# Kernel optimization log

Hardware: AMD Instinct MI355X
Metric: run time of the kernel (lower is better)

The kernel has to match this reference:

```python
import jax, jax.numpy as jnp
import numpy as np

# FIR kernel from resample_kernel=(1,3,3,1): outer product, normalized (gain=1)
_FIR_1D = np.array([1.0, 3.0, 3.0, 1.0], dtype=np.float32)
_FIR = np.outer(_FIR_1D, _FIR_1D)
_FIR = _FIR / _FIR.sum()  # 4x4


def setup_inputs() -> dict:
    key = jax.random.key(0)
    k1, k2, k3 = jax.random.split(key, 3)
    x = jax.random.normal(k1, (16, 256, 64, 64), dtype=jnp.float32)
    # fan_avg uniform init (default_init): variance = 1/fan_avg, fan_in=fan_out=256*9
    scale = float(np.sqrt(3.0 / (256 * 9)))
    w = jax.random.uniform(k2, (256, 256, 3, 3), dtype=jnp.float32, minval=-scale, maxval=scale)
    b = jax.random.normal(k3, (256,), dtype=jnp.float32) * 0.01
    return {"x": x, "w": w, "b": b}


def reference(x, w, b):
    # conv_downsample_2d: upfirdn2d(x, k, pad=(2,2)) then conv2d stride 2, then + bias
    B, C, H, W = x.shape
    # upfirdn2d with up=1, down=1 == zero-padded true convolution with k.
    # k is symmetric so flip is a no-op, but keep it for faithfulness.
    fir = jnp.asarray(_FIR[::-1, ::-1])                       # [4,4]
    fir_k = jnp.tile(fir[None, None, :, :], (C, 1, 1, 1))     # [C,1,4,4] depthwise
    x = jax.lax.conv_general_dilated(
        x, fir_k,
        window_strides=(1, 1),
        padding=((2, 2), (2, 2)),                             # (p+1)//2, p//2 with p=4
        feature_group_count=C,
        dimension_numbers=("NCHW", "OIHW", "NCHW"),
    )                                                          # [B,C,H+1,W+1]
    y = jax.lax.conv_general_dilated(
        x, w,
        window_strides=(2, 2),
        padding="VALID",
        dimension_numbers=("NCHW", "OIHW", "NCHW"),
    )                                                          # [B,outC,H//2,W//2]
    return y + b[None, :, None, None]
```

## Files before the change

### kernel.cpp

```cpp
#include <hip/hip_runtime.h>
#include <hip/hip_bf16.h>

typedef __attribute__((ext_vector_type(8))) short bf16x8;
typedef __attribute__((ext_vector_type(4))) float f32x4;
typedef __attribute__((ext_vector_type(8))) unsigned short u16x8;

#define KD 2304
#define PL 4232
#define OUT_PER_B (256 * 1024)

static __device__ __forceinline__ ushort f2bf(float f) {
  union { float f; unsigned int i; } v; v.f = f;
  unsigned int x = v.i;
  x += 0x7fffu + ((x >> 16) & 1u);
  return (ushort)(x >> 16);
}

#define GLDS16(gp, lp)                                                         \
  __builtin_amdgcn_global_load_lds(                                            \
      (const __attribute__((address_space(1))) void*)(gp),                     \
      (__attribute__((address_space(3))) void*)(lp), 16, 0, 0)

__global__ __launch_bounds__(256) void k_fir(const float* __restrict__ x,
                                             ushort* __restrict__ xfn) {
  __shared__ float sxp[64 * 76];
  __shared__ float stp[68 * 68];
  const int plane = blockIdx.x;
  const float* xp = x + (size_t)plane * 4096;
  ushort* op = xfn + (size_t)plane * PL;
  const int t = threadIdx.x;

  {
    int r = t & 63, cs = t >> 6;
    int col = (cs < 2) ? (2 + cs) : (66 + cs);
    sxp[r * 76 + col] = 0.f;
  }
  for (int i = t; i < 272; i += 256) {
    int rr = i / 68, cc = i - rr * 68;
    int row = (rr < 2) ? rr : (64 + rr);
    stp[row * 68 + cc] = 0.f;
  }

  const float4* x4 = (const float4*)xp;
#pragma unroll
  for (int i = 0; i < 4; ++i) {
    int f4 = t + 256 * i;
    int r = f4 >> 4, w4 = f4 & 15;
    *(float4*)&sxp[r * 76 + 4 + w4 * 4] = x4[f4];
  }
  __syncthreads();

  for (int g = t; g < 1088; g += 256) {
    int i = g / 17, jg = g - i * 17;
    int j0 = jg << 2;
    const float* s = &sxp[i * 76 + j0];
    float4 a0 = *(const float4*)(s);
    float4 a1 = *(const float4*)(s + 4);
    float4 a2 = *(const float4*)(s + 8);
    float4 o;
    o.x = (a0.z + a1.y) + 3.f * (a0.w + a1.x);
    o.y = (a0.w + a1.z) + 3.f * (a1.x + a1.y);
    o.z = (a1.x + a1.w) + 3.f * (a1.y + a1.z);
    o.w = (a1.y + a2.x) + 3.f * (a1.z + a1.w);
    *(float4*)&stp[(i + 2) * 68 + j0] = o;
  }
  __syncthreads();

  for (int g = t; g < 1105; g += 256) {
    int i = g / 17, jg = g - i * 17;
    int j0 = jg << 2;
    const float* s = &stp[i * 68 + j0];
    float4 r0 = *(const float4*)(s);
    float4 r1 = *(const float4*)(s + 68);
    float4 r2 = *(const float4*)(s + 136);
    float4 r3 = *(const float4*)(s + 204);
    float4 o;
    o.x = (r0.x + r3.x) + 3.f * (r1.x + r2.x);
    o.y = (r0.y + r3.y) + 3.f * (r1.y + r2.y);
    o.z = (r0.z + r3.z) + 3.f * (r1.z + r2.z);
    o.w = (r0.w + r3.w) + 3.f * (r1.w + r2.w);
    ushort* q = op + i * 65 + j0;
    q[0] = f2bf(o.x * 0.015625f);
    if (j0 + 1 < 65) q[1] = f2bf(o.y * 0.015625f);
    if (j0 + 2 < 65) q[2] = f2bf(o.z * 0.015625f);
    if (j0 + 3 < 65) q[3] = f2bf(o.w * 0.015625f);
  }
}

__global__ __launch_bounds__(256) void k_tr(const ushort* __restrict__ xfn,
                                            ushort* __restrict__ xft) {
  __shared__ ushort ld[128 * 66];
  const int hw0 = blockIdx.x * 128;
  const int c0 = blockIdx.y * 64;
  const int b = blockIdx.z;
  const int t = threadIdx.x;

#pragma unroll
  for (int it = 0; it < 4; ++it) {
    int idx = it * 256 + t;
    int c = idx >> 4, q = idx & 15;
    u16x8 v = {};
    if (hw0 + q * 8 < 4225)
      v = *(const u16x8*)(xfn + (size_t)(b * 256 + c0 + c) * PL + hw0 + q * 8);
#pragma unroll
    for (int k = 0; k < 8; ++k)
      ld[(q * 8 + k) * 66 + (c ^ (k << 3))] = v[k];
  }
  __syncthreads();
#pragma unroll
  for (int it = 0; it < 4; ++it) {
    int idx = it * 256 + t;
    int hwl = idx >> 3, a = idx & 7;
    int k7 = hwl & 7;
    int hw = hw0 + hwl;
    if (hw < 4225) {
      u16x8 v = *(const u16x8*)&ld[hwl * 66 + ((a ^ k7) << 3)];
      *(u16x8*)&xft[((size_t)(b * 4225 + hw) << 8) + c0 + (a << 3)] = v;
    }
  }
}

__global__ __launch_bounds__(256) void k_wcast2(const float* __restrict__ w,
                                                ushort* __restrict__ wb) {
  int iw = blockIdx.x * 256 + threadIdx.x;
  float v = w[iw];
  int j = iw % 9;
  int t2 = iw / 9;
  int ic = t2 & 255;
  int oc = t2 >> 8;
  wb[oc * KD + j * 256 + ic] = f2bf(v);
}

__global__ __launch_bounds__(256) void k_gemm3(const ushort* __restrict__ Wb,
                                               const ushort* __restrict__ Xt,
                                               const float* __restrict__ bias,
                                               float* __restrict__ out) {
  __shared__ ushort lA[128 * 64];
  __shared__ ushort lB[64 * 64];
  const int bid = blockIdx.x;
  const int work = (bid & 7) * 64 + (bid >> 3);
  const int ntile = work >> 1;
  const int mtile = work & 1;
  const int m0 = mtile * 128;
  const int n0 = ntile * 64;
  const int t = threadIdx.x;
  const int wid = t >> 6, lane = t & 63;
  const int wm = wid >> 1, wn = wid & 1;
  const int lrow = lane & 15, kgrp = lane >> 4;
  const int sw = lrow & 7;

  const ushort* aB[4];
#pragma unroll
  for (int i = 0; i < 4; ++i) {
    int idx = i * 256 + t;
    int row = idx >> 3;
    aB[i] = Wb + (size_t)(m0 + row) * KD + (((idx & 7) ^ (row & 7)) << 3);
  }
  const ushort* bB[2];
#pragma unroll
  for (int i = 0; i < 2; ++i) {
    int idx = i * 256 + t;
    int row = idx >> 3;
    int n = n0 + row;
    int b = n >> 10, oh = (n >> 5) & 31, ow = n & 31;
    bB[i] = Xt + ((size_t)((b * 65 + 2 * oh) * 65 + 2 * ow) << 8) +
            (((idx & 7) ^ (row & 7)) << 3);
  }

  f32x4 acc[4][2];
#pragma unroll
  for (int i = 0; i < 4; ++i)
#pragma unroll
    for (int j = 0; j < 2; ++j) acc[i][j] = (f32x4){0.f, 0.f, 0.f, 0.f};

  const int cA0 = ((kgrp ^ sw) << 3);
  const int cA1 = (((kgrp + 4) ^ sw) << 3);

  for (int kt = 0; kt < 36; ++kt) {
    const int j = kt >> 2;
    const int dh = j / 3, dw = j - 3 * dh;
    const int boff = (dh * 65 + dw) * 256 + ((kt & 3) << 6);
    const int k0 = kt << 6;
    __syncthreads();
#pragma unroll
    for (int i = 0; i < 4; ++i)
      GLDS16(aB[i] + k0, &lA[(i * 256 + t) * 8]);
#pragma unroll
    for (int i = 0; i < 2; ++i)
      GLDS16(bB[i] + boff, &lB[(i * 256 + t) * 8]);
    __syncthreads();

    bf16x8 Af[4][2], Bf[2][2];
#pragma unroll
    for (int f = 0; f < 4; ++f) {
      int row = wm * 64 + f * 16 + lrow;
      Af[f][0] = *(const bf16x8*)&lA[row * 64 + cA0];
      Af[f][1] = *(const bf16x8*)&lA[row * 64 + cA1];
    }
#pragma unroll
    for (int f = 0; f < 2; ++f) {
      int row = wn * 32 + f * 16 + lrow;
      Bf[f][0] = *(const bf16x8*)&lB[row * 64 + cA0];
      Bf[f][1] = *(const bf16x8*)&lB[row * 64 + cA1];
    }
#pragma unroll
    for (int h = 0; h < 2; ++h)
#pragma unroll
      for (int fm = 0; fm < 4; ++fm)
#pragma unroll
        for (int fn = 0; fn < 2; ++fn)
          acc[fm][fn] = __builtin_amdgcn_mfma_f32_16x16x32_bf16(
              Af[fm][h], Bf[fn][h], acc[fm][fn], 0, 0, 0);
  }

  f32x4 bv[4];
#pragma unroll
  for (int fm = 0; fm < 4; ++fm)
    bv[fm] = *(const f32x4*)(bias + m0 + wm * 64 + fm * 16 + kgrp * 4);

#pragma unroll
  for (int fm = 0; fm < 4; ++fm) {
#pragma unroll
    for (int fn = 0; fn < 2; ++fn) {
      int nn = n0 + wn * 32 + fn * 16 + lrow;
      int oc = m0 + wm * 64 + fm * 16 + kgrp * 4;
      float* op = out + (size_t)(nn >> 10) * OUT_PER_B + (nn & 1023) +
                  (size_t)oc * 1024;
      op[0]    = acc[fm][fn][0] + bv[fm][0];
      op[1024] = acc[fm][fn][1] + bv[fm][1];
      op[2048] = acc[fm][fn][2] + bv[fm][2];
      op[3072] = acc[fm][fn][3] + bv[fm][3];
    }
  }
}

extern "C" void kernel_launch(void* const* d_in, const int* in_sizes, int n_in,
                              void* d_out, int out_size, void* d_ws, size_t ws_size,
                              hipStream_t stream) {
  const float* x    = (const float*)d_in[0];
  const float* w    = (const float*)d_in[1];
  const float* bias = (const float*)d_in[2];
  float* out = (float*)d_out;

  char* ws = (char*)d_ws;
  ushort* xfn = (ushort*)ws;
  ushort* xft = (ushort*)(ws + 34668544);
  ushort* wb  = (ushort*)(ws + 34668544 + 34611200);

  k_fir<<<4096, 256, 0, stream>>>(x, xfn);
  k_tr<<<dim3(34, 4, 16), 256, 0, stream>>>(xfn, xft);
  k_wcast2<<<2304, 256, 0, stream>>>(w, wb);
  k_gemm3<<<512, 256, 0, stream>>>(wb, xft, bias, out);
}
```

Before: 73.89 us.

## Double-buffer GEMM LDS tiles with async prefetch and fuse weight cast into FIR

```diff
diff --git a/kernel.cpp b/kernel.cpp
--- a/kernel.cpp
+++ b/kernel.cpp
@@ -21,14 +21,31 @@
       (const __attribute__((address_space(1))) void*)(gp),                     \
       (__attribute__((address_space(3))) void*)(lp), 16, 0, 0)
 
+#define LDSOFF(p) ((unsigned)(size_t)(__attribute__((address_space(3))) const void*)(p))
+
+#define DSREAD(dst, addr) \
+  asm volatile("ds_read_b128 %0, %1" : "=v"(dst) : "v"(addr))
+
 __global__ __launch_bounds__(256) void k_fir(const float* __restrict__ x,
-                                             ushort* __restrict__ xfn) {
+                                             ushort* __restrict__ xfn,
+                                             const float* __restrict__ w,
+                                             ushort* __restrict__ wb) {
   __shared__ float sxp[64 * 76];
   __shared__ float stp[68 * 68];
   const int plane = blockIdx.x;
   const float* xp = x + (size_t)plane * 4096;
   ushort* op = xfn + (size_t)plane * PL;
   const int t = threadIdx.x;
+
+  if (plane < 2304) {
+    int iw = plane * 256 + t;
+    float v = w[iw];
+    int j = iw % 9;
+    int t2 = iw / 9;
+    int ic = t2 & 255;
+    int oc = t2 >> 8;
+    wb[oc * KD + j * 256 + ic] = f2bf(v);
+  }
 
   {
     int r = t & 63, cs = t >> 6;
@@ -120,23 +137,12 @@
   }
 }
 
-__global__ __launch_bounds__(256) void k_wcast2(const float* __restrict__ w,
-                                                ushort* __restrict__ wb) {
-  int iw = blockIdx.x * 256 + threadIdx.x;
-  float v = w[iw];
-  int j = iw % 9;
-  int t2 = iw / 9;
-  int ic = t2 & 255;
-  int oc = t2 >> 8;
-  wb[oc * KD + j * 256 + ic] = f2bf(v);
-}
-
 __global__ __launch_bounds__(256) void k_gemm3(const ushort* __restrict__ Wb,
                                                const ushort* __restrict__ Xt,
                                                const float* __restrict__ bias,
                                                float* __restrict__ out) {
-  __shared__ ushort lA[128 * 64];
-  __shared__ ushort lB[64 * 64];
+  __shared__ ushort lA[2][128 * 64];
+  __shared__ ushort lB[2][64 * 64];
   const int bid = blockIdx.x;
   const int work = (bid & 7) * 64 + (bid >> 3);
   const int ntile = work >> 1;
@@ -147,7 +153,6 @@
   const int wid = t >> 6, lane = t & 63;
   const int wm = wid >> 1, wn = wid & 1;
   const int lrow = lane & 15, kgrp = lane >> 4;
-  const int sw = lrow & 7;
 
   const ushort* aB[4];
 #pragma unroll
@@ -167,50 +172,81 @@
             (((idx & 7) ^ (row & 7)) << 3);
   }
 
+#define STAGE(buf, kt)                                                         \
+  {                                                                            \
+    const int j_ = (kt) >> 2;                                                  \
+    const int dh_ = j_ / 3, dw_ = j_ - 3 * dh_;                                \
+    const int boff_ = (dh_ * 65 + dw_) * 256 + (((kt) & 3) << 6);              \
+    const int k0_ = (kt) << 6;                                                 \
+    _Pragma("unroll") for (int i_ = 0; i_ < 4; ++i_)                           \
+        GLDS16(aB[i_] + k0_, &lA[buf][(i_ * 256 + t) * 8]);                    \
+    _Pragma("unroll") for (int i_ = 0; i_ < 2; ++i_)                           \
+        GLDS16(bB[i_] + boff_, &lB[buf][(i_ * 256 + t) * 8]);                  \
+  }
+
+  unsigned aAddr[2][4], bAddr[2][2];
+#pragma unroll
+  for (int f = 0; f < 4; ++f) {
+    int row = wm * 64 + f * 16 + lrow;
+#pragma unroll
+    for (int s = 0; s < 2; ++s) {
+      int col = ((s * 4 + kgrp) ^ row) & 7;
+      aAddr[s][f] = LDSOFF(&lA[0][row * 64 + col * 8]);
+    }
+  }
+#pragma unroll
+  for (int f = 0; f < 2; ++f) {
+    int row = wn * 32 + f * 16 + lrow;
+#pragma unroll
+    for (int s = 0; s < 2; ++s) {
+      int col = ((s * 4 + kgrp) ^ row) & 7;
+      bAddr[s][f] = LDSOFF(&lB[0][row * 64 + col * 8]);
+    }
+  }
+
   f32x4 acc[4][2];
 #pragma unroll
   for (int i = 0; i < 4; ++i)
 #pragma unroll
     for (int j = 0; j < 2; ++j) acc[i][j] = (f32x4){0.f, 0.f, 0.f, 0.f};
 
-  const int cA0 = ((kgrp ^ sw) << 3);
-  const int cA1 = (((kgrp + 4) ^ sw) << 3);
+  STAGE(0, 0);
 
   for (int kt = 0; kt < 36; ++kt) {
-    const int j = kt >> 2;
-    const int dh = j / 3, dw = j - 3 * dh;
-    const int boff = (dh * 65 + dw) * 256 + ((kt & 3) << 6);
-    const int k0 = kt << 6;
-    __syncthreads();
-#pragma unroll
-    for (int i = 0; i < 4; ++i)
-      GLDS16(aB[i] + k0, &lA[(i * 256 + t) * 8]);
-#pragma unroll
-    for (int i = 0; i < 2; ++i)
-      GLDS16(bB[i] + boff, &lB[(i * 256 + t) * 8]);
-    __syncthreads();
-
-    bf16x8 Af[4][2], Bf[2][2];
-#pragma unroll
-    for (int f = 0; f < 4; ++f) {
-      int row = wm * 64 + f * 16 + lrow;
-      Af[f][0] = *(const bf16x8*)&lA[row * 64 + cA0];
-      Af[f][1] = *(const bf16x8*)&lA[row * 64 + cA1];
-    }
-#pragma unroll
-    for (int f = 0; f < 2; ++f) {
-      int row = wn * 32 + f * 16 + lrow;
-      Bf[f][0] = *(const bf16x8*)&lB[row * 64 + cA0];
-      Bf[f][1] = *(const bf16x8*)&lB[row * 64 + cA1];
-    }
-#pragma unroll
-    for (int h = 0; h < 2; ++h)
-#pragma unroll
-      for (int fm = 0; fm < 4; ++fm)
-#pragma unroll
-        for (int fn = 0; fn < 2; ++fn)
-          acc[fm][fn] = __builtin_amdgcn_mfma_f32_16x16x32_bf16(
-              Af[fm][h], Bf[fn][h], acc[fm][fn], 0, 0, 0);
+    const int cur = kt & 1;
+    if (kt < 35) STAGE(cur ^ 1, kt + 1);
+
+    if (kt < 35)
+      asm volatile("s_waitcnt vmcnt(6)" ::: "memory");
+    else
+      asm volatile("s_waitcnt vmcnt(0)" ::: "memory");
+    __builtin_amdgcn_s_barrier();
+    __builtin_amdgcn_sched_barrier(0);
+
+    const unsigned oA = cur ? (unsigned)(128 * 64 * 2) : 0u;
+    const unsigned oB = cur ? (unsigned)(64 * 64 * 2) : 0u;
+#pragma unroll
+    for (int s = 0; s < 2; ++s) {
+      bf16x8 Af0, Af1, Af2, Af3, Bf0, Bf1;
+      DSREAD(Af0, aAddr[s][0] + oA);
+      DSREAD(Af1, aAddr[s][1] + oA);
+      DSREAD(Af2, aAddr[s][2] + oA);
+      DSREAD(Af3, aAddr[s][3] + oA);
+      DSREAD(Bf0, bAddr[s][0] + oB);
+      DSREAD(Bf1, bAddr[s][1] + oB);
+      asm volatile("s_waitcnt lgkmcnt(0)" ::: "memory");
+      __builtin_amdgcn_sched_barrier(0);
+      acc[0][0] = __builtin_amdgcn_mfma_f32_16x16x32_bf16(Af0, Bf0, acc[0][0], 0, 0, 0);
+      acc[0][1] = __builtin_amdgcn_mfma_f32_16x16x32_bf16(Af0, Bf1, acc[0][1], 0, 0, 0);
+      acc[1][0] = __builtin_amdgcn_mfma_f32_16x16x32_bf16(Af1, Bf0, acc[1][0], 0, 0, 0);
+      acc[1][1] = __builtin_amdgcn_mfma_f32_16x16x32_bf16(Af1, Bf1, acc[1][1], 0, 0, 0);
+      acc[2][0] = __builtin_amdgcn_mfma_f32_16x16x32_bf16(Af2, Bf0, acc[2][0], 0, 0, 0);
+      acc[2][1] = __builtin_amdgcn_mfma_f32_16x16x32_bf16(Af2, Bf1, acc[2][1], 0, 0, 0);
+      acc[3][0] = __builtin_amdgcn_mfma_f32_16x16x32_bf16(Af3, Bf0, acc[3][0], 0, 0, 0);
+      acc[3][1] = __builtin_amdgcn_mfma_f32_16x16x32_bf16(Af3, Bf1, acc[3][1], 0, 0, 0);
+    }
+    __builtin_amdgcn_sched_barrier(0);
+    __builtin_amdgcn_s_barrier();
   }
 
   f32x4 bv[4];
@@ -247,8 +283,7 @@
   ushort* xft = (ushort*)(ws + 34668544);
   ushort* wb  = (ushort*)(ws + 34668544 + 34611200);
 
-  k_fir<<<4096, 256, 0, stream>>>(x, xfn);
+  k_fir<<<4096, 256, 0, stream>>>(x, xfn, w, wb);
   k_tr<<<dim3(34, 4, 16), 256, 0, stream>>>(xfn, xft);
-  k_wcast2<<<2304, 256, 0, stream>>>(w, wb);
   k_gemm3<<<512, 256, 0, stream>>>(wb, xft, bias, out);
 }
```

Result: faster. 70.08 us (-5.2%).
